# Kernel tuning notes

Measured on AMD Instinct MI355X. Metric: run time of the kernel, lower is better.

Reference implementation:

```python
import jax, jax.numpy as jnp
import numpy as np
import math

B, S, HID = 2, 2048, 1024
NUM_HEADS = 16
HEAD_DIM = HID // NUM_HEADS
SPARSITY_RATIO = 0.1
NEG = -1e9


def _make_sparse_mask(key, seq_len, sparsity_ratio):
    # local window: min(32, seq_len // 4), rows attend to |i - j| <= window // 2
    local_window = min(32, seq_len // 4)
    half = local_window // 2
    idx = jnp.arange(seq_len)
    mask = jnp.abs(idx[:, None] - idx[None, :]) <= half  # [S, S] bool
    # random global connections: n_global random columns per row
    n_global = int(seq_len * sparsity_ratio)
    gidx = jax.random.randint(key, (seq_len, n_global), 0, seq_len)
    mask = mask.at[idx[:, None], gidx].set(True)
    return mask


def setup_inputs() -> dict:
    key = jax.random.key(0)
    ks = jax.random.split(key, 6)
    lim = math.sqrt(6.0 / (HID + HID))  # xavier uniform bound
    def w(k):
        return jax.random.uniform(k, (HID, HID), jnp.float32, -lim, lim)
    return {
        "hidden_states": jax.random.normal(ks[0], (B, S, HID), jnp.float32),
        "Wq": w(ks[1]), "bq": jnp.zeros((HID,), jnp.float32),
        "Wk": w(ks[2]), "bk": jnp.zeros((HID,), jnp.float32),
        "Wv": w(ks[3]), "bv": jnp.zeros((HID,), jnp.float32),
        "Wo": w(ks[4]), "bo": jnp.zeros((HID,), jnp.float32),
        "sparse_mask": _make_sparse_mask(ks[5], S, SPARSITY_RATIO),
    }


def reference(hidden_states, Wq, bq, Wk, bk, Wv, bv, Wo, bo, sparse_mask):
    Bsz, seq, hid = hidden_states.shape
    H, D = NUM_HEADS, hid // NUM_HEADS

    def proj(W, b):
        y = hidden_states @ W.T + b                      # [B, S, hid]
        return y.reshape(Bsz, seq, H, D).transpose(0, 2, 1, 3)  # [B, H, S, D]

    q = proj(Wq, bq)
    k = proj(Wk, bk)
    v = proj(Wv, bv)

    scores = jnp.einsum("bhqd,bhkd->bhqk", q, k) / jnp.sqrt(jnp.float32(D))
    scores = jnp.where(sparse_mask[None, None, :, :], scores, jnp.float32(NEG))
    probs = jax.nn.softmax(scores, axis=-1)
    ctx = jnp.einsum("bhqk,bhkd->bhqd", probs, v)        # [B, H, S, D]
    ctx = ctx.transpose(0, 2, 1, 3).reshape(Bsz, seq, hid)
    return ctx @ Wo.T + bo
```

## Files before the change

### kernel.cpp

```cpp
#include <hip/hip_runtime.h>

typedef short bf16x8 __attribute__((ext_vector_type(8)));
typedef short bf16x4 __attribute__((ext_vector_type(4)));
typedef float f32x4 __attribute__((ext_vector_type(4)));
typedef unsigned short us4 __attribute__((ext_vector_type(4)));

#define S_LEN 2048
#define HIDD 1024
#define NH 16
#define HD 64

#define BK 64

static __device__ __forceinline__ unsigned short f2bf(float f) {
  union { float f; unsigned u; } v; v.f = f;
  unsigned r = v.u + 0x7FFFu + ((v.u >> 16) & 1u);
  return (unsigned short)(r >> 16);
}

static __device__ __forceinline__ float bf2f(unsigned short u) {
  union { unsigned u; float f; } v; v.u = ((unsigned)u) << 16;
  return v.f;
}

static __device__ __forceinline__ unsigned cvtpk(float lo, float hi) {
  unsigned r;
  asm("v_cvt_pk_bf16_f32 %0, %1, %2" : "=v"(r) : "v"(lo), "v"(hi));
  return r;
}

static __device__ __forceinline__ float ex2(float x) {
#if __has_builtin(__builtin_amdgcn_exp2f)
  return __builtin_amdgcn_exp2f(x);
#else
  return __expf(x * 0.69314718056f);
#endif
}

static __device__ __forceinline__ f32x4 mfma16(bf16x4 a, bf16x4 b, f32x4 c) {
#if __has_builtin(__builtin_amdgcn_mfma_f32_16x16x16bf16_1k)
  return __builtin_amdgcn_mfma_f32_16x16x16bf16_1k(a, b, c, 0, 0, 0);
#else
  asm("v_mfma_f32_16x16x16_bf16 %0, %1, %2, %0" : "+v"(c) : "v"(a), "v"(b));
  return c;
#endif
}

#define GLD16(gp, lp)                                                        \
  __builtin_amdgcn_global_load_lds(                                         \
      (const __attribute__((address_space(1))) void*)(gp),                  \
      (__attribute__((address_space(3))) void*)(lp), 16, 0, 0)

__global__ __launch_bounds__(256) void cvt5_kernel(
    const float* __restrict__ s0, const float* __restrict__ s1, const float* __restrict__ s2,
    const float* __restrict__ s3, const float* __restrict__ s4,
    unsigned short* __restrict__ d0, unsigned short* __restrict__ d1,
    unsigned short* __restrict__ d2, unsigned short* __restrict__ d3,
    unsigned short* __restrict__ d4) {
  const float* s; unsigned short* d; int n4;
  switch (blockIdx.y) {
    case 0: s = s0; d = d0; n4 = (2 * S_LEN * HIDD) / 4; break;
    case 1: s = s1; d = d1; n4 = (HIDD * HIDD) / 4; break;
    case 2: s = s2; d = d2; n4 = (HIDD * HIDD) / 4; break;
    case 3: s = s3; d = d3; n4 = (HIDD * HIDD) / 4; break;
    default: s = s4; d = d4; n4 = (HIDD * HIDD) / 4; break;
  }
  for (int i = blockIdx.x * blockDim.x + threadIdx.x; i < n4;
       i += gridDim.x * blockDim.x) {
    float4 v = ((const float4*)s)[i];
    us4 o;
    o.x = f2bf(v.x); o.y = f2bf(v.y); o.z = f2bf(v.z); o.w = f2bf(v.w);
    ((us4*)d)[i] = o;
  }
}

__global__ __launch_bounds__(256) void maskbits_kernel(
    const unsigned char* __restrict__ m8, unsigned* __restrict__ bits) {
  int idx = blockIdx.x * 256 + threadIdx.x;
  int q = idx >> 6, w = idx & 63;
  bool bytemode = (m8[1] != 0);
  unsigned r = 0;
  if (bytemode) {
    const uint4* p = (const uint4*)(m8 + (size_t)q * 2048 + w * 32);
    uint4 a = p[0], b = p[1];
    unsigned v[8] = {a.x, a.y, a.z, a.w, b.x, b.y, b.z, b.w};
#pragma unroll
    for (int j = 0; j < 8; ++j)
#pragma unroll
      for (int k = 0; k < 4; ++k)
        r |= (((v[j] >> (k * 8)) & 255u) ? 1u : 0u) << (j * 4 + k);
  } else {
    const int4* p = (const int4*)((const int*)m8 + (size_t)q * 2048 + (size_t)w * 32);
#pragma unroll
    for (int j = 0; j < 8; ++j) {
      int4 v = p[j];
      r |= (v.x ? 1u : 0u) << (j * 4 + 0);
      r |= (v.y ? 1u : 0u) << (j * 4 + 1);
      r |= (v.z ? 1u : 0u) << (j * 4 + 2);
      r |= (v.w ? 1u : 0u) << (j * 4 + 3);
    }
  }
  bits[idx] = r;
}

template <int MFRAG>
static __device__ __forceinline__ void gemm_core2(
    const unsigned short* __restrict__ A, const unsigned short* __restrict__ W,
    int bm0, int bn0, unsigned short* As, unsigned short* Bs,
    f32x4 (&acc)[MFRAG][4]) {
  const int tid = threadIdx.x;
  const int lane = tid & 63;
  const int wid = tid >> 6;
  const int wr = wid >> 1, wc = wid & 1;
  const int l15 = lane & 15, g = lane >> 4, l7 = l15 & 7;
  const int ra = (g ^ l7) * 8;

  for (int k0 = 0; k0 < HIDD; k0 += BK) {
    __syncthreads();
#pragma unroll
    for (int it = 0; it < MFRAG; ++it) {
      int p = it * 256 + tid;
      int r = p >> 3, ch = (p & 7) ^ (r & 7);
      GLD16(A + (size_t)(bm0 + r) * HIDD + k0 + ch * 8,
            As + (it * 256 + wid * 64) * 8);
    }
#pragma unroll
    for (int it = 0; it < 4; ++it) {
      int p = it * 256 + tid;
      int r = p >> 3, ch = (p & 7) ^ (r & 7);
      GLD16(W + (size_t)(bn0 + r) * HIDD + k0 + ch * 8,
            Bs + (it * 256 + wid * 64) * 8);
    }
    __syncthreads();
#pragma unroll
    for (int kk = 0; kk < 2; ++kk) {
      bf16x8 af[MFRAG], bfr[4];
#pragma unroll
      for (int m = 0; m < MFRAG; ++m)
        af[m] = *(const bf16x8*)&As[(wr * (MFRAG * 16) + m * 16 + l15) * 64 + (ra ^ (kk * 32))];
#pragma unroll
      for (int n = 0; n < 4; ++n)
        bfr[n] = *(const bf16x8*)&Bs[(wc * 64 + n * 16 + l15) * 64 + (ra ^ (kk * 32))];
#pragma unroll
      for (int m = 0; m < MFRAG; ++m)
#pragma unroll
        for (int n = 0; n < 4; ++n)
          acc[m][n] = __builtin_amdgcn_mfma_f32_16x16x32_bf16(af[m], bfr[n], acc[m][n], 0, 0, 0);
    }
  }
}

__global__ __launch_bounds__(256) void gemm_qkv(
    const unsigned short* __restrict__ hs,
    const unsigned short* __restrict__ Wq, const unsigned short* __restrict__ Wk,
    const unsigned short* __restrict__ Wv,
    const float* __restrict__ bq, const float* __restrict__ bk, const float* __restrict__ bv,
    unsigned short* __restrict__ Qs, unsigned short* __restrict__ Kb,
    unsigned short* __restrict__ VT) {
  __shared__ __align__(16) unsigned short As[128 * 64];
  __shared__ __align__(16) unsigned short Bs[128 * 64];
  const int z = blockIdx.z;
  const unsigned short* W = (z == 0) ? Wq : ((z == 1) ? Wk : Wv);
  const float* bias = (z == 0) ? bq : ((z == 1) ? bk : bv);

  f32x4 acc[4][4];
#pragma unroll
  for (int m = 0; m < 4; ++m)
#pragma unroll
    for (int n = 0; n < 4; ++n) acc[m][n] = (f32x4){0.f, 0.f, 0.f, 0.f};

  const int bm0 = blockIdx.x * 128, bn0 = blockIdx.y * 128;
  gemm_core2<4>(hs, W, bm0, bn0, As, Bs, acc);

  const int lane = threadIdx.x & 63;
  const int wid = threadIdx.x >> 6;
  const int wr = wid >> 1, wc = wid & 1;
  const int l15 = lane & 15, g = lane >> 4;
  const float qscale = 0.125f * 1.44269504088896f;

#pragma unroll
  for (int m = 0; m < 4; ++m) {
#pragma unroll
    for (int n = 0; n < 4; ++n) {
      int grow0 = bm0 + wr * 64 + m * 16 + g * 4;
      int gcol = bn0 + wc * 64 + n * 16 + l15;
      float bv_ = bias[gcol];
      if (z == 0) {
#pragma unroll
        for (int i = 0; i < 4; ++i)
          Qs[(size_t)(grow0 + i) * HIDD + gcol] = f2bf((acc[m][n][i] + bv_) * qscale);
      } else if (z == 1) {
#pragma unroll
        for (int i = 0; i < 4; ++i)
          Kb[(size_t)(grow0 + i) * HIDD + gcol] = f2bf(acc[m][n][i] + bv_);
      } else {
        int b = grow0 >> 11, s = grow0 & 2047;
        int h = gcol >> 6, d = gcol & 63;
        us4 pk;
#pragma unroll
        for (int i = 0; i < 4; ++i) pk[i] = f2bf(acc[m][n][i] + bv_);
        *(us4*)&VT[((size_t)(b * NH + h) * HD + d) * S_LEN + s] = pk;
      }
    }
  }
}

__global__ __launch_bounds__(256) void gemm_o(
    const unsigned short* __restrict__ ctx, const unsigned short* __restrict__ Wo,
    const float* __restrict__ bo, float* __restrict__ out) {
  __shared__ __align__(16) unsigned short As[64 * 64];
  __shared__ __align__(16) unsigned short Bs[128 * 64];
  f32x4 acc[2][4];
#pragma unroll
  for (int m = 0; m < 2; ++m)
#pragma unroll
    for (int n = 0; n < 4; ++n) acc[m][n] = (f32x4){0.f, 0.f, 0.f, 0.f};

  const int bm0 = blockIdx.x * 64, bn0 = blockIdx.y * 128;
  gemm_core2<2>(ctx, Wo, bm0, bn0, As, Bs, acc);

  const int lane = threadIdx.x & 63;
  const int wid = threadIdx.x >> 6;
  const int wr = wid >> 1, wc = wid & 1;
  const int l15 = lane & 15, g = lane >> 4;
#pragma unroll
  for (int m = 0; m < 2; ++m) {
#pragma unroll
    for (int n = 0; n < 4; ++n) {
      int grow0 = bm0 + wr * 32 + m * 16 + g * 4;
      int gcol = bn0 + wc * 64 + n * 16 + l15;
      float bv_ = bo[gcol];
#pragma unroll
      for (int i = 0; i < 4; ++i)
        out[(size_t)(grow0 + i) * HIDD + gcol] = acc[m][n][i] + bv_;
    }
  }
}

__global__ __launch_bounds__(512, 4) void attn7_kernel(
    const unsigned short* __restrict__ Qs, const unsigned short* __restrict__ Kb,
    const unsigned short* __restrict__ VT, const unsigned* __restrict__ mbits,
    unsigned short* __restrict__ part0, unsigned short* __restrict__ part1,
    float2* __restrict__ ml) {
  __shared__ __align__(16) unsigned short Kt[2][4096];
  __shared__ __align__(16) unsigned short Vt[2][4096];

  const int tid = threadIdx.x;
  const int wid = tid >> 6, lane = tid & 63;
  const int l15 = lane & 15, g = lane >> 4;
  const int l7 = l15 & 7;
  const int b = blockIdx.x >> 4, h = blockIdx.x & 15;
  const int z = blockIdx.z;
  const int kvbase = z * 1024;
  const int qrow = blockIdx.y * 128 + wid * 16 + l15;

  const unsigned short* Kbh = Kb + (size_t)b * S_LEN * HIDD + h * HD;
  const unsigned short* VTbh = VT + (size_t)(b * NH + h) * HD * S_LEN;

  const unsigned short* Qrow = Qs + (size_t)(b * S_LEN + qrow) * HIDD + h * HD;
  bf16x8 qf0 = *(const bf16x8*)(Qrow + g * 8);
  bf16x8 qf1 = *(const bf16x8*)(Qrow + 32 + g * 8);

  const unsigned* mrow = mbits + (size_t)qrow * 64 + z * 32;

  const int rb0 = l15 * 64 + (g ^ l7) * 8;
  const int rb1 = l15 * 64 + ((g ^ l7) ^ 4) * 8;

  const int gh = g >> 1, gl = g & 1;
  int vta[4];
#pragma unroll
  for (int t = 0; t < 4; ++t)
    vta[t] = l15 * 64 + (((2 * t + gh) ^ l7) * 8) + gl * 4;

  const bool isK = (wid < 4);
  const int wk = wid & 3;
  int p0 = wk * 128 + lane;
  int p1 = p0 + 64;
  int r0 = p0 >> 3, c0 = (p0 & 7) ^ (r0 & 7);
  int r1 = p1 >> 3, c1 = (p1 & 7) ^ (r1 & 7);
  const unsigned short* gp0;
  const unsigned short* gp1;
  int gstep;
  unsigned short* lp0;
  if (isK) {
    gp0 = Kbh + (size_t)(kvbase + r0) * HIDD + c0 * 8;
    gp1 = Kbh + (size_t)(kvbase + r1) * HIDD + c1 * 8;
    gstep = 64 * HIDD;
    lp0 = &Kt[0][0] + wk * 1024;
  } else {
    gp0 = VTbh + (size_t)r0 * S_LEN + kvbase + c0 * 8;
    gp1 = VTbh + (size_t)r1 * S_LEN + kvbase + c1 * 8;
    gstep = 64;
    lp0 = &Vt[0][0] + wk * 1024;
  }
  unsigned short* lp1 = lp0 + 512;

  float m_run = -1e8f, l_run = 0.f;
  f32x4 oacc[4];
#pragma unroll
  for (int dc = 0; dc < 4; ++dc) oacc[dc] = (f32x4){0.f, 0.f, 0.f, 0.f};

  GLD16(gp0, lp0);
  GLD16(gp1, lp1);
  gp0 += gstep; gp1 += gstep;
  uint2 mw = *(const uint2*)mrow;
  int kt = 0;
  __syncthreads();

#define ABODY(BUF)                                                            \
  {                                                                           \
    GLD16(gp0, lp0 + ((BUF) ^ 1) * 4096);                                     \
    GLD16(gp1, lp1 + ((BUF) ^ 1) * 4096);                                     \
    gp0 += gstep; gp1 += gstep;                                               \
    uint2 mw_n = *(const uint2*)(mrow + (kt + 1) * 2);   \
    f32x4 sacc[4];                                                            \
    _Pragma("unroll")                                                         \
    for (int t = 0; t < 4; ++t) {                                             \
      sacc[t] = (f32x4){0.f, 0.f, 0.f, 0.f};                                  \
      bf16x8 ka = *(const bf16x8*)&Kt[BUF][t * 1024 + rb0];                   \
      bf16x8 kb2 = *(const bf16x8*)&Kt[BUF][t * 1024 + rb1];                  \
      sacc[t] = __builtin_amdgcn_mfma_f32_16x16x32_bf16(ka, qf0, sacc[t], 0, 0, 0); \
      sacc[t] = __builtin_amdgcn_mfma_f32_16x16x32_bf16(kb2, qf1, sacc[t], 0, 0, 0); \
    }                                                                         \
    float t0 = fmaxf(fmaxf(sacc[0][0], sacc[0][1]), sacc[0][2]);              \
    float t1 = fmaxf(fmaxf(sacc[0][3], sacc[1][0]), sacc[1][1]);              \
    float t2 = fmaxf(fmaxf(sacc[1][2], sacc[1][3]), sacc[2][0]);              \
    float t3 = fmaxf(fmaxf(sacc[2][1], sacc[2][2]), sacc[2][3]);              \
    float t4 = fmaxf(fmaxf(sacc[3][0], sacc[3][1]), sacc[3][2]);              \
    float t5 = fmaxf(fmaxf(t0, t1), sacc[3][3]);                              \
    float pmax = fmaxf(fmaxf(fmaxf(t2, t3), t4), t5);                         \
    pmax = fmaxf(pmax, __shfl_xor(pmax, 16));                                 \
    pmax = fmaxf(pmax, __shfl_xor(pmax, 32));                                 \
    if (__any(pmax > m_run + 8.0f)) {                                         \
      float m_new = fmaxf(m_run, pmax);                                       \
      float corr = ex2(m_run - m_new);                                        \
      l_run *= corr;                                                          \
      _Pragma("unroll")                                                       \
      for (int dc = 0; dc < 4; ++dc) oacc[dc] *= corr;                        \
      m_run = m_new;                                                          \
    }                                                                         \
    float lsum = 0.f;                                                         \
    bf16x4 pb[4];                                                             \
    _Pragma("unroll")                                                         \
    for (int t = 0; t < 4; ++t) {                                             \
      unsigned word = (t & 2) ? mw.y : mw.x;                                  \
      unsigned nib = word >> ((t & 1) * 16 + g * 4);                          \
      float e0 = ex2(sacc[t][0] - m_run);                                     \
      float e1 = ex2(sacc[t][1] - m_run);                                     \
      float e2 = ex2(sacc[t][2] - m_run);                                     \
      float e3 = ex2(sacc[t][3] - m_run);                                     \
      float q0 = (nib & 1u) ? e0 : 0.f;                                       \
      float q1 = (nib & 2u) ? e1 : 0.f;                                       \
      float q2 = (nib & 4u) ? e2 : 0.f;                                       \
      float q3 = (nib & 8u) ? e3 : 0.f;                                       \
      lsum += (q0 + q1) + (q2 + q3);                                          \
      union { unsigned u[2]; bf16x4 v; } pu;                                  \
      pu.u[0] = cvtpk(q0, q1);                                                \
      pu.u[1] = cvtpk(q2, q3);                                                \
      pb[t] = pu.v;                                                           \
    }                                                                         \
    lsum += __shfl_xor(lsum, 16);                                             \
    lsum += __shfl_xor(lsum, 32);                                             \
    l_run += lsum;                                                            \
    _Pragma("unroll")                                                         \
    for (int dc = 0; dc < 4; ++dc) {                                          \
      f32x4 o = oacc[dc];                                                     \
      _Pragma("unroll")                                                       \
      for (int t = 0; t < 4; ++t) {                                           \
        bf16x4 va = *(const bf16x4*)&Vt[BUF][vta[t] + dc * 1024];             \
        o = mfma16(va, pb[t], o);                                             \
      }                                                                       \
      oacc[dc] = o;                                                           \
    }                                                                         \
    mw = mw_n;                                                                \
    ++kt;                                                                     \
    __syncthreads();                                                          \
  }

  for (int h8 = 0; h8 < 8; ++h8) {
    ABODY(0);
    ABODY(1);
  }
#undef ABODY

  float linv = 1.f / fmaxf(l_run, 1e-37f);
  unsigned short* obase = (z == 0) ? part0 : part1;
  unsigned short* crow = obase + (size_t)(b * S_LEN + qrow) * HIDD + h * HD;
#pragma unroll
  for (int dc = 0; dc < 4; ++dc) {
    uint2 o;
    o.x = cvtpk(oacc[dc][0] * linv, oacc[dc][1] * linv);
    o.y = cvtpk(oacc[dc][2] * linv, oacc[dc][3] * linv);
    *(uint2*)&crow[dc * 16 + g * 4] = o;
  }
  if (g == 0) {
    ml[(size_t)z * (32 * S_LEN) + (size_t)blockIdx.x * S_LEN + qrow] =
        make_float2(m_run, l_run);
  }
}

__global__ __launch_bounds__(256) void combine_kernel(
    const unsigned short* p1, const float2* __restrict__ ml,
    unsigned short* p0 ) {
  int gid = blockIdx.x * 256 + threadIdx.x;
  int r = gid >> 2;
  int dq = (gid & 3) * 16;
  float2 a = ml[r];
  float2 c = ml[65536 + r];
  float m = fmaxf(a.x, c.x);
  float w0 = a.y * ex2(a.x - m);
  float w1 = c.y * ex2(c.x - m);
  float inv = 1.f / (w0 + w1);
  w0 *= inv; w1 *= inv;
  int bh = r >> 11, q = r & 2047;
  int b = bh >> 4, h = bh & 15;
  size_t off = ((size_t)(b * S_LEN + q)) * HIDD + h * HD + dq;
#pragma unroll
  for (int half = 0; half < 2; ++half) {
    bf16x8 o0 = *(const bf16x8*)(p0 + off + half * 8);
    bf16x8 o1 = *(const bf16x8*)(p1 + off + half * 8);
    unsigned res[4];
#pragma unroll
    for (int j = 0; j < 4; ++j) {
      float v0 = w0 * bf2f((unsigned short)o0[2 * j]) + w1 * bf2f((unsigned short)o1[2 * j]);
      float v1 = w0 * bf2f((unsigned short)o0[2 * j + 1]) + w1 * bf2f((unsigned short)o1[2 * j + 1]);
      res[j] = cvtpk(v0, v1);
    }
    uint4 st = {res[0], res[1], res[2], res[3]};
    *(uint4*)(p0 + off + half * 8) = st;
  }
}

extern "C" void kernel_launch(void* const* d_in, const int* in_sizes, int n_in,
                              void* d_out, int out_size, void* d_ws, size_t ws_size,
                              hipStream_t stream) {
  const float* hs = (const float*)d_in[0];
  const float* Wq = (const float*)d_in[1];
  const float* bq = (const float*)d_in[2];
  const float* Wk = (const float*)d_in[3];
  const float* bk = (const float*)d_in[4];
  const float* Wv = (const float*)d_in[5];
  const float* bv = (const float*)d_in[6];
  const float* Wo = (const float*)d_in[7];
  const float* bo = (const float*)d_in[8];
  const unsigned char* mask = (const unsigned char*)d_in[9];

  char* ws = (char*)d_ws;
  unsigned short* hs_bf = (unsigned short*)(ws);
  unsigned short* Wq_bf = (unsigned short*)(ws + (8u << 20));
  unsigned short* Wk_bf = (unsigned short*)(ws + (10u << 20));
  unsigned short* Wv_bf = (unsigned short*)(ws + (12u << 20));
  unsigned short* Wo_bf = (unsigned short*)(ws + (14u << 20));
  unsigned short* Qs    = (unsigned short*)(ws + (16u << 20));
  unsigned short* Kbf   = (unsigned short*)(ws + (24u << 20));
  unsigned short* VT    = (unsigned short*)(ws + (32u << 20));
  unsigned short* ctxb  = (unsigned short*)(ws + (40u << 20));
  unsigned* mbits       = (unsigned*)(ws);
  unsigned short* part1 = (unsigned short*)(ws + (1u << 19));
  float2* ml            = (float2*)(ws + (9u << 20));
  float* out = (float*)d_out;

  cvt5_kernel<<<dim3(256, 5), 256, 0, stream>>>(hs, Wq, Wk, Wv, Wo,
                                                hs_bf, Wq_bf, Wk_bf, Wv_bf, Wo_bf);
  gemm_qkv<<<dim3(32, 8, 3), 256, 0, stream>>>(hs_bf, Wq_bf, Wk_bf, Wv_bf,
                                               bq, bk, bv, Qs, Kbf, VT);
  maskbits_kernel<<<512, 256, 0, stream>>>(mask, mbits);
  attn7_kernel<<<dim3(32, 16, 2), 512, 0, stream>>>(Qs, Kbf, VT, mbits,
                                                    ctxb, part1, ml);
  combine_kernel<<<1024, 256, 0, stream>>>(part1, ml, ctxb);
  gemm_o<<<dim3(64, 8), 256, 0, stream>>>(ctxb, Wo_bf, bo, out);
}
```

Baseline: 148.9 us.

## Process two query tiles per wave to reuse K/V shared-memory loads

Each wave now handles two 16-row query tiles instead of one, so each block covers 256 query rows and the grid's y dimension is halved. Every K and V fragment read from shared memory feeds two MFMA chains, which halves the global K/V traffic per query and the LDS reads per MFMA. The online-softmax code moves into a helper that runs once per tile. The cost is roughly double the accumulator and score registers per thread, which may cut occupancy under launch_bounds(512,4), and there are only half as many blocks to spread across the CUs.

```diff
diff --git a/kernel.cpp b/kernel.cpp
--- a/kernel.cpp
+++ b/kernel.cpp
@@ -237,7 +237,55 @@
   }
 }
 
-__global__ __launch_bounds__(512, 4) void attn7_kernel(
+static __device__ __forceinline__ float max16(const f32x4 (&s)[4]) {
+  float t0 = fmaxf(fmaxf(s[0][0], s[0][1]), s[0][2]);
+  float t1 = fmaxf(fmaxf(s[0][3], s[1][0]), s[1][1]);
+  float t2 = fmaxf(fmaxf(s[1][2], s[1][3]), s[2][0]);
+  float t3 = fmaxf(fmaxf(s[2][1], s[2][2]), s[2][3]);
+  float t4 = fmaxf(fmaxf(s[3][0], s[3][1]), s[3][2]);
+  float t5 = fmaxf(fmaxf(t0, t1), s[3][3]);
+  return fmaxf(fmaxf(fmaxf(t2, t3), t4), t5);
+}
+
+static __device__ __forceinline__ void softmax_tile(
+    const f32x4 (&s)[4], float& m_run, float& l_run, f32x4 (&oacc)[4],
+    uint2 mw, int g, bf16x4 (&pb)[4]) {
+  float pmax = max16(s);
+  pmax = fmaxf(pmax, __shfl_xor(pmax, 16));
+  pmax = fmaxf(pmax, __shfl_xor(pmax, 32));
+  if (__any(pmax > m_run + 8.0f)) {
+    float m_new = fmaxf(m_run, pmax);
+    float corr = ex2(m_run - m_new);
+    l_run *= corr;
+#pragma unroll
+    for (int dc = 0; dc < 4; ++dc) oacc[dc] *= corr;
+    m_run = m_new;
+  }
+  float lsum = 0.f;
+#pragma unroll
+  for (int t = 0; t < 4; ++t) {
+    unsigned word = (t & 2) ? mw.y : mw.x;
+    unsigned nib = word >> ((t & 1) * 16 + g * 4);
+    float e0 = ex2(s[t][0] - m_run);
+    float e1 = ex2(s[t][1] - m_run);
+    float e2 = ex2(s[t][2] - m_run);
+    float e3 = ex2(s[t][3] - m_run);
+    float q0 = (nib & 1u) ? e0 : 0.f;
+    float q1 = (nib & 2u) ? e1 : 0.f;
+    float q2 = (nib & 4u) ? e2 : 0.f;
+    float q3 = (nib & 8u) ? e3 : 0.f;
+    lsum += (q0 + q1) + (q2 + q3);
+    union { unsigned u[2]; bf16x4 v; } pu;
+    pu.u[0] = cvtpk(q0, q1);
+    pu.u[1] = cvtpk(q2, q3);
+    pb[t] = pu.v;
+  }
+  lsum += __shfl_xor(lsum, 16);
+  lsum += __shfl_xor(lsum, 32);
+  l_run += lsum;
+}
+
+__global__ __launch_bounds__(512, 4) void attn8_kernel(
     const unsigned short* __restrict__ Qs, const unsigned short* __restrict__ Kb,
     const unsigned short* __restrict__ VT, const unsigned* __restrict__ mbits,
     unsigned short* __restrict__ part0, unsigned short* __restrict__ part1,
@@ -252,16 +300,21 @@
   const int b = blockIdx.x >> 4, h = blockIdx.x & 15;
   const int z = blockIdx.z;
   const int kvbase = z * 1024;
-  const int qrow = blockIdx.y * 128 + wid * 16 + l15;
+  const int qrowA = blockIdx.y * 256 + wid * 32 + l15;
+  const int qrowB = qrowA + 16;
 
   const unsigned short* Kbh = Kb + (size_t)b * S_LEN * HIDD + h * HD;
   const unsigned short* VTbh = VT + (size_t)(b * NH + h) * HD * S_LEN;
 
-  const unsigned short* Qrow = Qs + (size_t)(b * S_LEN + qrow) * HIDD + h * HD;
-  bf16x8 qf0 = *(const bf16x8*)(Qrow + g * 8);
-  bf16x8 qf1 = *(const bf16x8*)(Qrow + 32 + g * 8);
-
-  const unsigned* mrow = mbits + (size_t)qrow * 64 + z * 32;
+  const unsigned short* QrowA = Qs + (size_t)(b * S_LEN + qrowA) * HIDD + h * HD;
+  const unsigned short* QrowB = Qs + (size_t)(b * S_LEN + qrowB) * HIDD + h * HD;
+  bf16x8 qfA0 = *(const bf16x8*)(QrowA + g * 8);
+  bf16x8 qfA1 = *(const bf16x8*)(QrowA + 32 + g * 8);
+  bf16x8 qfB0 = *(const bf16x8*)(QrowB + g * 8);
+  bf16x8 qfB1 = *(const bf16x8*)(QrowB + 32 + g * 8);
+
+  const unsigned* mrowA = mbits + (size_t)qrowA * 64 + z * 32;
+  const unsigned* mrowB = mbits + (size_t)qrowB * 64 + z * 32;
 
   const int rb0 = l15 * 64 + (g ^ l7) * 8;
   const int rb1 = l15 * 64 + ((g ^ l7) ^ 4) * 8;
@@ -295,15 +348,20 @@
   }
   unsigned short* lp1 = lp0 + 512;
 
-  float m_run = -1e8f, l_run = 0.f;
-  f32x4 oacc[4];
-#pragma unroll
-  for (int dc = 0; dc < 4; ++dc) oacc[dc] = (f32x4){0.f, 0.f, 0.f, 0.f};
+  float m_runA = -1e8f, l_runA = 0.f;
+  float m_runB = -1e8f, l_runB = 0.f;
+  f32x4 oaccA[4], oaccB[4];
+#pragma unroll
+  for (int dc = 0; dc < 4; ++dc) {
+    oaccA[dc] = (f32x4){0.f, 0.f, 0.f, 0.f};
+    oaccB[dc] = (f32x4){0.f, 0.f, 0.f, 0.f};
+  }
 
   GLD16(gp0, lp0);
   GLD16(gp1, lp1);
   gp0 += gstep; gp1 += gstep;
-  uint2 mw = *(const uint2*)mrow;
+  uint2 mwA = *(const uint2*)mrowA;
+  uint2 mwB = *(const uint2*)mrowB;
   int kt = 0;
   __syncthreads();
 
@@ -312,67 +370,34 @@
     GLD16(gp0, lp0 + ((BUF) ^ 1) * 4096);                                     \
     GLD16(gp1, lp1 + ((BUF) ^ 1) * 4096);                                     \
     gp0 += gstep; gp1 += gstep;                                               \
-    uint2 mw_n = *(const uint2*)(mrow + (kt + 1) * 2);   \
-    f32x4 sacc[4];                                                            \
+    uint2 mwA_n = *(const uint2*)(mrowA + (kt + 1) * 2);      \
+    uint2 mwB_n = *(const uint2*)(mrowB + (kt + 1) * 2);                      \
+    f32x4 sA[4], sB[4];                                                       \
     _Pragma("unroll")                                                         \
     for (int t = 0; t < 4; ++t) {                                             \
-      sacc[t] = (f32x4){0.f, 0.f, 0.f, 0.f};                                  \
       bf16x8 ka = *(const bf16x8*)&Kt[BUF][t * 1024 + rb0];                   \
       bf16x8 kb2 = *(const bf16x8*)&Kt[BUF][t * 1024 + rb1];                  \
-      sacc[t] = __builtin_amdgcn_mfma_f32_16x16x32_bf16(ka, qf0, sacc[t], 0, 0, 0); \
-      sacc[t] = __builtin_amdgcn_mfma_f32_16x16x32_bf16(kb2, qf1, sacc[t], 0, 0, 0); \
+      f32x4 zz = (f32x4){0.f, 0.f, 0.f, 0.f};                                 \
+      sA[t] = __builtin_amdgcn_mfma_f32_16x16x32_bf16(ka, qfA0, zz, 0, 0, 0); \
+      sA[t] = __builtin_amdgcn_mfma_f32_16x16x32_bf16(kb2, qfA1, sA[t], 0, 0, 0); \
+      sB[t] = __builtin_amdgcn_mfma_f32_16x16x32_bf16(ka, qfB0, zz, 0, 0, 0); \
+      sB[t] = __builtin_amdgcn_mfma_f32_16x16x32_bf16(kb2, qfB1, sB[t], 0, 0, 0); \
     }                                                                         \
-    float t0 = fmaxf(fmaxf(sacc[0][0], sacc[0][1]), sacc[0][2]);              \
-    float t1 = fmaxf(fmaxf(sacc[0][3], sacc[1][0]), sacc[1][1]);              \
-    float t2 = fmaxf(fmaxf(sacc[1][2], sacc[1][3]), sacc[2][0]);              \
-    float t3 = fmaxf(fmaxf(sacc[2][1], sacc[2][2]), sacc[2][3]);              \
-    float t4 = fmaxf(fmaxf(sacc[3][0], sacc[3][1]), sacc[3][2]);              \
-    float t5 = fmaxf(fmaxf(t0, t1), sacc[3][3]);                              \
-    float pmax = fmaxf(fmaxf(fmaxf(t2, t3), t4), t5);                         \
-    pmax = fmaxf(pmax, __shfl_xor(pmax, 16));                                 \
-    pmax = fmaxf(pmax, __shfl_xor(pmax, 32));                                 \
-    if (__any(pmax > m_run + 8.0f)) {                                         \
-      float m_new = fmaxf(m_run, pmax);                                       \
-      float corr = ex2(m_run - m_new);                                        \
-      l_run *= corr;                                                          \
-      _Pragma("unroll")                                                       \
-      for (int dc = 0; dc < 4; ++dc) oacc[dc] *= corr;                        \
-      m_run = m_new;                                                          \
-    }                                                                         \
-    float lsum = 0.f;                                                         \
-    bf16x4 pb[4];                                                             \
-    _Pragma("unroll")                                                         \
-    for (int t = 0; t < 4; ++t) {                                             \
-      unsigned word = (t & 2) ? mw.y : mw.x;                                  \
-      unsigned nib = word >> ((t & 1) * 16 + g * 4);                          \
-      float e0 = ex2(sacc[t][0] - m_run);                                     \
-      float e1 = ex2(sacc[t][1] - m_run);                                     \
-      float e2 = ex2(sacc[t][2] - m_run);                                     \
-      float e3 = ex2(sacc[t][3] - m_run);                                     \
-      float q0 = (nib & 1u) ? e0 : 0.f;                                       \
-      float q1 = (nib & 2u) ? e1 : 0.f;                                       \
-      float q2 = (nib & 4u) ? e2 : 0.f;                                       \
-      float q3 = (nib & 8u) ? e3 : 0.f;                                       \
-      lsum += (q0 + q1) + (q2 + q3);                                          \
-      union { unsigned u[2]; bf16x4 v; } pu;                                  \
-      pu.u[0] = cvtpk(q0, q1);                                                \
-      pu.u[1] = cvtpk(q2, q3);                                                \
-      pb[t] = pu.v;                                                           \
-    }                                                                         \
-    lsum += __shfl_xor(lsum, 16);                                             \
-    lsum += __shfl_xor(lsum, 32);                                             \
-    l_run += lsum;                                                            \
+    bf16x4 pbA[4], pbB[4];                                                    \
+    softmax_tile(sA, m_runA, l_runA, oaccA, mwA, g, pbA);                     \
+    softmax_tile(sB, m_runB, l_runB, oaccB, mwB, g, pbB);                     \
     _Pragma("unroll")                                                         \
     for (int dc = 0; dc < 4; ++dc) {                                          \
-      f32x4 o = oacc[dc];                                                     \
+      f32x4 oA = oaccA[dc], oB = oaccB[dc];                                   \
       _Pragma("unroll")                                                       \
       for (int t = 0; t < 4; ++t) {                                           \
         bf16x4 va = *(const bf16x4*)&Vt[BUF][vta[t] + dc * 1024];             \
-        o = mfma16(va, pb[t], o);                                             \
+        oA = mfma16(va, pbA[t], oA);                                          \
+        oB = mfma16(va, pbB[t], oB);                                          \
       }                                                                       \
-      oacc[dc] = o;                                                           \
+      oaccA[dc] = oA; oaccB[dc] = oB;                                         \
     }                                                                         \
-    mw = mw_n;                                                                \
+    mwA = mwA_n; mwB = mwB_n;                                                 \
     ++kt;                                                                     \
     __syncthreads();                                                          \
   }
@@ -383,19 +408,34 @@
   }
 #undef ABODY
 
-  float linv = 1.f / fmaxf(l_run, 1e-37f);
   unsigned short* obase = (z == 0) ? part0 : part1;
-  unsigned short* crow = obase + (size_t)(b * S_LEN + qrow) * HIDD + h * HD;
-#pragma unroll
-  for (int dc = 0; dc < 4; ++dc) {
-    uint2 o;
-    o.x = cvtpk(oacc[dc][0] * linv, oacc[dc][1] * linv);
-    o.y = cvtpk(oacc[dc][2] * linv, oacc[dc][3] * linv);
-    *(uint2*)&crow[dc * 16 + g * 4] = o;
+  {
+    float linv = 1.f / fmaxf(l_runA, 1e-37f);
+    unsigned short* crow = obase + (size_t)(b * S_LEN + qrowA) * HIDD + h * HD;
+#pragma unroll
+    for (int dc = 0; dc < 4; ++dc) {
+      uint2 o;
+      o.x = cvtpk(oaccA[dc][0] * linv, oaccA[dc][1] * linv);
+      o.y = cvtpk(oaccA[dc][2] * linv, oaccA[dc][3] * linv);
+      *(uint2*)&crow[dc * 16 + g * 4] = o;
+    }
+  }
+  {
+    float linv = 1.f / fmaxf(l_runB, 1e-37f);
+    unsigned short* crow = obase + (size_t)(b * S_LEN + qrowB) * HIDD + h * HD;
+#pragma unroll
+    for (int dc = 0; dc < 4; ++dc) {
+      uint2 o;
+      o.x = cvtpk(oaccB[dc][0] * linv, oaccB[dc][1] * linv);
+      o.y = cvtpk(oaccB[dc][2] * linv, oaccB[dc][3] * linv);
+      *(uint2*)&crow[dc * 16 + g * 4] = o;
+    }
   }
   if (g == 0) {
-    ml[(size_t)z * (32 * S_LEN) + (size_t)blockIdx.x * S_LEN + qrow] =
-        make_float2(m_run, l_run);
+    ml[(size_t)z * (32 * S_LEN) + (size_t)blockIdx.x * S_LEN + qrowA] =
+        make_float2(m_runA, l_runA);
+    ml[(size_t)z * (32 * S_LEN) + (size_t)blockIdx.x * S_LEN + qrowB] =
+        make_float2(m_runB, l_runB);
   }
 }
 
@@ -465,8 +505,8 @@
   gemm_qkv<<<dim3(32, 8, 3), 256, 0, stream>>>(hs_bf, Wq_bf, Wk_bf, Wv_bf,
                                                bq, bk, bv, Qs, Kbf, VT);
   maskbits_kernel<<<512, 256, 0, stream>>>(mask, mbits);
-  attn7_kernel<<<dim3(32, 16, 2), 512, 0, stream>>>(Qs, Kbf, VT, mbits,
-                                                    ctxb, part1, ml);
+  attn8_kernel<<<dim3(32, 8, 2), 512, 0, stream>>>(Qs, Kbf, VT, mbits,
+                                                   ctxb, part1, ml);
   combine_kernel<<<1024, 256, 0, stream>>>(part1, ml, ctxb);
   gemm_o<<<dim3(64, 8), 256, 0, stream>>>(ctxb, Wo_bf, bo, out);
 }
```

New measurement: 148.0 us. Within noise of the previous version (-0.6%).
